# Kernel tuning notes

Hardware: AMD Instinct MI355X
Metric: run time of the kernel (lower is better)

Reference implementation:

```python
import jax, jax.numpy as jnp
import numpy as np

EMBED_DIM = 768
NUM_HEADS = 12
HEAD_DIM = EMBED_DIM // NUM_HEADS
SCALE = HEAD_DIM ** -0.5
B, N = 8, 1024


def setup_inputs() -> dict:
    key = jax.random.key(0)
    ks = jax.random.split(key, 5)
    return {
        "x": jax.random.normal(ks[0], (B, N, EMBED_DIM), dtype=jnp.float32),
        "qkv_w": jax.random.normal(ks[1], (3 * EMBED_DIM, EMBED_DIM), dtype=jnp.float32) * 0.02,
        "qkv_b": jax.random.normal(ks[2], (3 * EMBED_DIM,), dtype=jnp.float32) * 0.02,
        "proj_w": jax.random.normal(ks[3], (EMBED_DIM, EMBED_DIM), dtype=jnp.float32) * 0.02,
        "proj_b": jax.random.normal(ks[4], (EMBED_DIM,), dtype=jnp.float32) * 0.02,
    }


def reference(x, qkv_w, qkv_b, proj_w, proj_b):
    b, n, c = x.shape
    h, hd = NUM_HEADS, HEAD_DIM
    # QKV projection: [b,n,3c]
    qkv = jnp.einsum("bnc,dc->bnd", x, qkv_w) + qkv_b
    qkv = qkv.reshape(b, n, 3, h, hd).transpose(2, 0, 3, 1, 4)  # [3,b,h,n,hd]
    q, k, v = qkv[0], qkv[1], qkv[2]
    # scaled dot-product attention (eager path; dropout is identity in eval)
    attn = jnp.einsum("bhqd,bhkd->bhqk", q, k) * SCALE
    attn = jax.nn.softmax(attn, axis=-1)
    out = jnp.einsum("bhqk,bhkd->bhqd", attn, v)  # [b,h,n,hd]
    out = out.transpose(0, 2, 1, 3).reshape(b, n, c)
    # output projection
    return jnp.einsum("bnc,dc->bnd", out, proj_w) + proj_b
```

## Files before the change

kernel.cpp:

```cpp
#include <hip/hip_runtime.h>
#include <hip/hip_bf16.h>

typedef __attribute__((ext_vector_type(4))) float f32x4;
typedef __attribute__((ext_vector_type(16))) float f32x16;
typedef __attribute__((ext_vector_type(8))) short short8;
typedef unsigned short u16;

#define MFMA(a, b, c) __builtin_amdgcn_mfma_f32_16x16x32_bf16((a), (b), (c), 0, 0, 0)
#define MFMA32(a, b, c) __builtin_amdgcn_mfma_f32_32x32x16_bf16((a), (b), (c), 0, 0, 0)

#define WAITVM_BAR(N) do {                                          \
    asm volatile("s_waitcnt vmcnt(" #N ")" ::: "memory");           \
    __builtin_amdgcn_s_barrier();                                   \
    __builtin_amdgcn_sched_barrier(0);                              \
} while (0)
#define BAR2() do {                                                 \
    __builtin_amdgcn_sched_barrier(0);                              \
    __builtin_amdgcn_s_barrier();                                   \
    __builtin_amdgcn_sched_barrier(0);                              \
} while (0)

static constexpr int EMBED = 768;
static constexpr int NH = 12;
static constexpr int HD = 64;
static constexpr int BATCH = 8;
static constexpr int SEQ = 1024;

__device__ __forceinline__ u16 f2bu(float f) {
    __hip_bfloat16 h = __float2bfloat16(f);
    u16 u; __builtin_memcpy(&u, &h, 2); return u;
}
__device__ __forceinline__ float exp2a(float x) {
    float r; asm("v_exp_f32 %0, %1" : "=v"(r) : "v"(x)); return r;
}
__device__ __forceinline__ unsigned cvt_pk_bf16(float lo, float hi) {
    unsigned r; asm("v_cvt_pk_bf16_f32 %0, %1, %2" : "=v"(r) : "v"(lo), "v"(hi)); return r;
}
__device__ __forceinline__ float max3f(float a, float b, float c) {
    return fmaxf(fmaxf(a, b), c);
}
__device__ __forceinline__ void swap32(unsigned& a, unsigned& b) {
    asm volatile("v_permlane32_swap_b32 %0, %1" : "+v"(a), "+v"(b));
}
__device__ __forceinline__ short8 mk8(unsigned w0, unsigned w1, unsigned w2, unsigned w3) {
    union { unsigned u[4]; short8 s; } c;
    c.u[0] = w0; c.u[1] = w1; c.u[2] = w2; c.u[3] = w3;
    return c.s;
}

__global__ void cvt_all_k(const float* __restrict__ x, const float* __restrict__ w1,
                          const float* __restrict__ w2,
                          u16* __restrict__ xb, u16* __restrict__ wb, u16* __restrict__ pw) {
    const int n1 = BATCH * SEQ * EMBED;
    const int n2 = 3 * EMBED * EMBED;
    const int n3 = EMBED * EMBED;
    int i = (blockIdx.x * blockDim.x + threadIdx.x) * 4;
    const float* src; u16* dst;
    if (i < n1)            { src = x  + i;             dst = xb + i; }
    else if (i < n1 + n2)  { src = w1 + (i - n1);      dst = wb + (i - n1); }
    else if (i < n1+n2+n3) { src = w2 + (i - n1 - n2); dst = pw + (i - n1 - n2); }
    else return;
    float4 v = *reinterpret_cast<const float4*>(src);
    ushort4 o;
    o.x = f2bu(v.x); o.y = f2bu(v.y); o.z = f2bu(v.z); o.w = f2bu(v.w);
    *reinterpret_cast<ushort4*>(dst) = o;
}

template <int EPI>
__global__ __launch_bounds__(256)
void gemm_bt_k(const u16* __restrict__ A, const u16* __restrict__ Bw,
               const float* __restrict__ bias,
               u16* __restrict__ q_out, u16* __restrict__ k_out,
               u16* __restrict__ vt_out, float* __restrict__ f_out)
{
    __shared__ __attribute__((aligned(16))) char smem[65536];
    const int tid  = threadIdx.x;
    const int wave = tid >> 6, lane = tid & 63;
    const int hi   = lane >> 4, l15 = lane & 15;
    const int wr   = wave >> 1, wc = wave & 1;
    const int bm   = blockIdx.x, bn = blockIdx.y;

    f32x4 acc[4][4] = {};

    const size_t arow0 = (size_t)bm * 128;
    const size_t brow0 = (size_t)bn * 128;

    auto stage = [&](int buf, int kt) {
        char* Ab = smem + buf * 32768;
        char* Bb = Ab + 16384;
#pragma unroll
        for (int c = 0; c < 4; ++c) {
            int ck   = c * 4 + wave;
            int p    = ck * 1024 + lane * 16;
            int row  = p >> 7;
            int pcol = (p & 127) ^ ((row & 7) << 4);
            const u16* srcA = A  + (arow0 + row) * EMBED + kt + (pcol >> 1);
            const u16* srcB = Bw + (brow0 + row) * EMBED + kt + (pcol >> 1);
            __builtin_amdgcn_global_load_lds((const __attribute__((address_space(1))) void*)srcA,
                                             (__attribute__((address_space(3))) void*)(Ab + ck * 1024), 16, 0, 0);
            __builtin_amdgcn_global_load_lds((const __attribute__((address_space(1))) void*)srcB,
                                             (__attribute__((address_space(3))) void*)(Bb + ck * 1024), 16, 0, 0);
        }
    };

    auto comp = [&](const char* Ab, const char* Bb) {
#pragma unroll
        for (int kk = 0; kk < 2; ++kk) {
            short8 af[4], bf[4];
#pragma unroll
            for (int mi = 0; mi < 4; ++mi) {
                int R  = wr * 64 + mi * 16 + l15;
                int Cb = kk * 64 + hi * 16;
                af[mi] = *reinterpret_cast<const short8*>(Ab + R * 128 + (Cb ^ ((R & 7) << 4)));
            }
#pragma unroll
            for (int ni = 0; ni < 4; ++ni) {
                int R  = wc * 64 + ni * 16 + l15;
                int Cb = kk * 64 + hi * 16;
                bf[ni] = *reinterpret_cast<const short8*>(Bb + R * 128 + (Cb ^ ((R & 7) << 4)));
            }
#pragma unroll
            for (int mi = 0; mi < 4; ++mi)
#pragma unroll
                for (int ni = 0; ni < 4; ++ni)
                    acc[mi][ni] = MFMA(af[mi], bf[ni], acc[mi][ni]);
        }
    };

    const char* A0 = smem;
    const char* B0 = smem + 16384;
    const char* A1 = smem + 32768;
    const char* B1 = smem + 49152;

    stage(0, 0);
#pragma unroll
    for (int tt = 0; tt < 5; ++tt) {
        stage(1, (2 * tt + 1) * 64);
        WAITVM_BAR(8);
        comp(A0, B0);
        BAR2();
        stage(0, (2 * tt + 2) * 64);
        WAITVM_BAR(8);
        comp(A1, B1);
        BAR2();
    }
    stage(1, 11 * 64);
    WAITVM_BAR(8);
    comp(A0, B0);
    BAR2();
    WAITVM_BAR(0);
    comp(A1, B1);

#pragma unroll
    for (int mi = 0; mi < 4; ++mi) {
        int crow0 = bm * 128 + wr * 64 + mi * 16 + hi * 4;
#pragma unroll
        for (int ni = 0; ni < 4; ++ni) {
            int ccol = bn * 128 + wc * 64 + ni * 16 + l15;
            float bv = bias[ccol];
            if constexpr (EPI == 0) {
                int which = ccol / 768;
                int rem   = ccol - which * 768;
                int hh = rem >> 6, hd = rem & 63;
                int bb = crow0 >> 10, nn0 = crow0 & 1023;
                size_t bh = (size_t)(bb * NH + hh);
                if (which == 2) {
                    uint2 pk;
                    pk.x = cvt_pk_bf16(acc[mi][ni][0] + bv, acc[mi][ni][1] + bv);
                    pk.y = cvt_pk_bf16(acc[mi][ni][2] + bv, acc[mi][ni][3] + bv);
                    *reinterpret_cast<uint2*>(&vt_out[(bh * HD + hd) * SEQ + nn0]) = pk;
                } else if (which == 0) {
#pragma unroll
                    for (int r = 0; r < 4; ++r)
                        q_out[(bh * SEQ + nn0 + r) * HD + hd] =
                            f2bu((acc[mi][ni][r] + bv) * 0.18033688f);
                } else {
#pragma unroll
                    for (int r = 0; r < 4; ++r)
                        k_out[(bh * SEQ + nn0 + r) * HD + hd] = f2bu(acc[mi][ni][r] + bv);
                }
            } else {
#pragma unroll
                for (int r = 0; r < 4; ++r)
                    f_out[(size_t)(crow0 + r) * EMBED + ccol] = acc[mi][ni][r] + bv;
            }
        }
    }
}

__global__ __launch_bounds__(256, 3)
void attn_k(const u16* __restrict__ Q, const u16* __restrict__ K,
            const u16* __restrict__ Vt, u16* __restrict__ AO)
{
    __shared__ __attribute__((aligned(16))) u16 kv[3][8192];

    const int tid = threadIdx.x;
    const int w   = tid >> 6, lane = tid & 63;
    const int h   = lane >> 5, l31 = lane & 31;
    const int f   = blockIdx.x;
    const int xcd = f & 7, i = f >> 3;
    const int bh  = xcd * 12 + (i % 12);
    const int q0w = (i / 12) * 128 + w * 32;

    const u16* Qh = Q  + (size_t)bh * SEQ * HD;
    const u16* Kh = K  + (size_t)bh * SEQ * HD;
    const u16* Vh = Vt + (size_t)bh * HD * SEQ;

    short8 qf[4];
#pragma unroll
    for (int ds = 0; ds < 4; ++ds)
        qf[ds] = *reinterpret_cast<const short8*>(
            Qh + (size_t)(q0w + l31) * HD + ds * 16 + h * 8);
    __builtin_amdgcn_sched_barrier(0);

    const u16* sptr[4]; int doff[4]; int sadv[4];
#pragma unroll
    for (int c = 0; c < 4; ++c) {
        int ch = c * 4 + w;
        int mc = ch & 7;
        int p  = mc * 1024 + lane * 16;
        int row = p >> 7;
        int colb = (p & 127) ^ ((row & 7) << 4);
        if (ch < 8) { sptr[c] = Kh + (size_t)row * HD + (colb >> 1); sadv[c] = 64 * HD; doff[c] = mc * 512; }
        else        { sptr[c] = Vh + (size_t)row * SEQ + (colb >> 1); sadv[c] = 64;     doff[c] = 4096 + mc * 512; }
    }
    auto stage = [&](int buf, int t) {
#pragma unroll
        for (int c = 0; c < 4; ++c)
            __builtin_amdgcn_global_load_lds(
                (const __attribute__((address_space(1))) void*)(sptr[c] + (size_t)t * sadv[c]),
                (__attribute__((address_space(3))) void*)(&kv[buf][doff[c]]), 16, 0, 0);
    };

    stage(0, 0);
    stage(1, 1);

    f32x16 accO[2] = {};
    float m = 0.f, lp = 0.f;

    auto tile = [&](const u16* Kb, const u16* Vb, bool first) {
        f32x16 st[2] = {{0}, {0}};
        __builtin_amdgcn_s_setprio(1);
#pragma unroll
        for (int mf = 0; mf < 2; ++mf) {
            int R  = mf * 32 + l31;
            int sw = (R & 7) << 4;
#pragma unroll
            for (int ds = 0; ds < 4; ++ds) {
                short8 kf = *reinterpret_cast<const short8*>(
                    Kb + R * 64 + (((ds * 32 + h * 16) ^ sw) >> 1));
                st[mf] = MFMA32(kf, qf[ds], st[mf]);
            }
        }
        __builtin_amdgcn_s_setprio(0);

        float x0 = max3f(st[0][0],  st[0][1],  st[0][2]);
        float x1 = max3f(st[0][3],  st[0][4],  st[0][5]);
        float x2 = max3f(st[0][6],  st[0][7],  st[0][8]);
        float x3 = max3f(st[0][9],  st[0][10], st[0][11]);
        float x4 = max3f(st[0][12], st[0][13], st[0][14]);
        float x5 = max3f(st[0][15], st[1][0],  st[1][1]);
        float x6 = max3f(st[1][2],  st[1][3],  st[1][4]);
        float x7 = max3f(st[1][5],  st[1][6],  st[1][7]);
        float x8 = max3f(st[1][8],  st[1][9],  st[1][10]);
        float x9 = max3f(st[1][11], st[1][12], st[1][13]);
        float xa = fmaxf(st[1][14], st[1][15]);
        float y0 = max3f(x0, x1, x2);
        float y1 = max3f(x3, x4, x5);
        float y2 = max3f(x6, x7, x8);
        float y3 = fmaxf(x9, xa);
        float tm = fmaxf(max3f(y0, y1, y2), y3);
        tm = fmaxf(tm, __shfl_xor(tm, 32, 64));
        if (first) m = tm;

        unsigned pkw[2][8];
        float s0 = 0.f, s1 = 0.f;
#pragma unroll
        for (int mf = 0; mf < 2; ++mf)
#pragma unroll
            for (int p = 0; p < 8; ++p) {
                float e0 = exp2a(st[mf][2 * p]     - m);
                float e1 = exp2a(st[mf][2 * p + 1] - m);
                if (mf == 0) s0 += e0 + e1; else s1 += e0 + e1;
                pkw[mf][p] = cvt_pk_bf16(e0, e1);
            }
        lp += s0 + s1;

        short8 pb[4];
#pragma unroll
        for (int ks = 0; ks < 4; ++ks) {
            int mf = ks >> 1, b4 = (ks & 1) * 4;
            unsigned E0 = pkw[mf][b4 + 0], E1 = pkw[mf][b4 + 1];
            unsigned D0 = pkw[mf][b4 + 2], D1 = pkw[mf][b4 + 3];
            swap32(E0, D0);
            swap32(E1, D1);
            pb[ks] = mk8(E0, E1, D0, D1);
        }

        __builtin_amdgcn_s_setprio(1);
#pragma unroll
        for (int df = 0; df < 2; ++df) {
            int R  = df * 32 + l31;
            int sw = (R & 7) << 4;
#pragma unroll
            for (int ks = 0; ks < 4; ++ks) {
                short8 vf = *reinterpret_cast<const short8*>(
                    Vb + R * 64 + (((ks * 32 + h * 16) ^ sw) >> 1));
                accO[df] = MFMA32(vf, pb[ks], accO[df]);
            }
        }
        __builtin_amdgcn_s_setprio(0);

        if (!first && !__all(tm <= m + 8.f)) {
            float mn = fmaxf(m, tm);
            float s  = exp2a(m - mn);
            m = mn;
            lp *= s;
#pragma unroll
            for (int df = 0; df < 2; ++df)
#pragma unroll
                for (int r = 0; r < 16; ++r) accO[df][r] *= s;
        }
    };

    auto one = [&](int bc, int bs, int tn, bool ds, bool first) {
        asm volatile("s_waitcnt vmcnt(4)" ::: "memory");
        __builtin_amdgcn_s_barrier();
        __builtin_amdgcn_sched_barrier(0);
        if (ds) stage(bs, tn);
        tile(&kv[bc][0], &kv[bc][4096], first);
        __builtin_amdgcn_sched_barrier(0);
    };

    one(0, 2, 2, true, true);
    one(1, 0, 3, true, false);
    one(2, 1, 4, true, false);
    for (int g = 1; g < 5; ++g) {
        one(0, 2, 3 * g + 2, true, false);
        one(1, 0, 3 * g + 3, 3 * g + 3 <= 15, false);
        one(2, 1, 3 * g + 4, 3 * g + 4 <= 15, false);
    }
    asm volatile("s_waitcnt vmcnt(0)" ::: "memory");
    __builtin_amdgcn_s_barrier();
    __builtin_amdgcn_sched_barrier(0);
    tile(&kv[0][0], &kv[0][4096], false);

    lp += __shfl_xor(lp, 32, 64);
    float linv = 1.f / lp;
    const int bb = bh / NH, hh = bh - bb * NH;
    size_t rowb = ((size_t)bb * SEQ + q0w + l31) * EMBED + hh * HD;
#pragma unroll
    for (int df = 0; df < 2; ++df)
#pragma unroll
        for (int g = 0; g < 4; ++g) {
            float o0 = accO[df][4 * g + 0] * linv;
            float o1 = accO[df][4 * g + 1] * linv;
            float o2 = accO[df][4 * g + 2] * linv;
            float o3 = accO[df][4 * g + 3] * linv;
            uint2 pk;
            pk.x = cvt_pk_bf16(o0, o1);
            pk.y = cvt_pk_bf16(o2, o3);
            *reinterpret_cast<uint2*>(&AO[rowb + df * 32 + 8 * g + 4 * h]) = pk;
        }
}

extern "C" void kernel_launch(void* const* d_in, const int* in_sizes, int n_in,
                              void* d_out, int out_size, void* d_ws, size_t ws_size,
                              hipStream_t stream)
{
    const float* x      = (const float*)d_in[0];
    const float* qkv_w  = (const float*)d_in[1];
    const float* qkv_b  = (const float*)d_in[2];
    const float* proj_w = (const float*)d_in[3];
    const float* proj_b = (const float*)d_in[4];
    float* out = (float*)d_out;

    char* ws = (char*)d_ws;
    u16* xb  = (u16*)(ws);
    u16* wb  = (u16*)(ws + 12582912);
    u16* pw  = (u16*)(ws + 16121856);
    u16* qb  = (u16*)(ws + 17301504);
    u16* kb  = (u16*)(ws + 29884416);
    u16* vt  = (u16*)(ws + 42467328);
    u16* ao  = (u16*)(ws + 55050240);

    cvt_all_k<<<8448, 256, 0, stream>>>(x, qkv_w, proj_w, xb, wb, pw);

    gemm_bt_k<0><<<dim3(64, 18), 256, 0, stream>>>(xb, wb, qkv_b, qb, kb, vt, nullptr);
    attn_k<<<768, 256, 0, stream>>>(qb, kb, vt, ao);
    gemm_bt_k<1><<<dim3(64, 6), 256, 0, stream>>>(ao, pw, proj_b, nullptr, nullptr, nullptr, out);
}
```

Measured before the change: 103.9 us.

## Compute softmax row sums via MFMA with ones and precompute LDS offsets

Replaces the per-lane VALU accumulation of softmax denominators (and the cross-lane shuffle) with an extra MFMA that multiplies the bf16 probability fragments by a ones vector, so the row sum arrives in an accumulator. The initial running max is fixed at a constant rather than taken from the first tile, which removes the first-tile special case. Swizzled LDS read offsets in both the GEMM and attention kernels are hoisted out of the inner loops. The sum now uses bf16-rounded probabilities, which adds MFMA work per tile and changes rounding slightly.

```diff
diff --git a/kernel.cpp b/kernel.cpp
--- a/kernel.cpp
+++ b/kernel.cpp
@@ -103,22 +103,25 @@
         }
     };
 
-    auto comp = [&](const char* Ab, const char* Bb) {
+    const int sw_l = (l15 & 7) << 4;
+    int aoff[2], boff[2];
+#pragma unroll
+    for (int kk = 0; kk < 2; ++kk) {
+        int col = (kk * 64 + hi * 16) ^ sw_l;
+        aoff[kk] = (wr * 64 + l15) * 128 + col;
+        boff[kk] = (wc * 64 + l15) * 128 + col;
+    }
+
+    auto comp = [&](int buf) {
 #pragma unroll
         for (int kk = 0; kk < 2; ++kk) {
             short8 af[4], bf[4];
 #pragma unroll
-            for (int mi = 0; mi < 4; ++mi) {
-                int R  = wr * 64 + mi * 16 + l15;
-                int Cb = kk * 64 + hi * 16;
-                af[mi] = *reinterpret_cast<const short8*>(Ab + R * 128 + (Cb ^ ((R & 7) << 4)));
-            }
-#pragma unroll
-            for (int ni = 0; ni < 4; ++ni) {
-                int R  = wc * 64 + ni * 16 + l15;
-                int Cb = kk * 64 + hi * 16;
-                bf[ni] = *reinterpret_cast<const short8*>(Bb + R * 128 + (Cb ^ ((R & 7) << 4)));
-            }
+            for (int mi = 0; mi < 4; ++mi)
+                af[mi] = *reinterpret_cast<const short8*>(smem + buf * 32768 + aoff[kk] + mi * 2048);
+#pragma unroll
+            for (int ni = 0; ni < 4; ++ni)
+                bf[ni] = *reinterpret_cast<const short8*>(smem + buf * 32768 + 16384 + boff[kk] + ni * 2048);
 #pragma unroll
             for (int mi = 0; mi < 4; ++mi)
 #pragma unroll
@@ -126,30 +129,25 @@
                     acc[mi][ni] = MFMA(af[mi], bf[ni], acc[mi][ni]);
         }
     };
-
-    const char* A0 = smem;
-    const char* B0 = smem + 16384;
-    const char* A1 = smem + 32768;
-    const char* B1 = smem + 49152;
 
     stage(0, 0);
 #pragma unroll
     for (int tt = 0; tt < 5; ++tt) {
         stage(1, (2 * tt + 1) * 64);
         WAITVM_BAR(8);
-        comp(A0, B0);
+        comp(0);
         BAR2();
         stage(0, (2 * tt + 2) * 64);
         WAITVM_BAR(8);
-        comp(A1, B1);
+        comp(1);
         BAR2();
     }
     stage(1, 11 * 64);
     WAITVM_BAR(8);
-    comp(A0, B0);
+    comp(0);
     BAR2();
     WAITVM_BAR(0);
-    comp(A1, B1);
+    comp(1);
 
 #pragma unroll
     for (int mi = 0; mi < 4; ++mi) {
@@ -235,23 +233,31 @@
     stage(0, 0);
     stage(1, 1);
 
+    const int sw_l = (l31 & 7) << 4;
+    int koff[4];
+#pragma unroll
+    for (int ds = 0; ds < 4; ++ds)
+        koff[ds] = l31 * 128 + ((ds * 32 + h * 16) ^ sw_l);
+
+    union { unsigned u[4]; short8 s; } oc;
+    oc.u[0] = oc.u[1] = oc.u[2] = oc.u[3] = 0x3F803F80u;
+    const short8 ones8 = oc.s;
+
     f32x16 accO[2] = {};
-    float m = 0.f, lp = 0.f;
-
-    auto tile = [&](const u16* Kb, const u16* Vb, bool first) {
+    f32x16 lsum = {};
+    float m = 8.f;
+
+    auto tile = [&](int BC) {
+        const char* base = (const char*)kv + BC * 16384;
         f32x16 st[2] = {{0}, {0}};
         __builtin_amdgcn_s_setprio(1);
 #pragma unroll
-        for (int mf = 0; mf < 2; ++mf) {
-            int R  = mf * 32 + l31;
-            int sw = (R & 7) << 4;
+        for (int mf = 0; mf < 2; ++mf)
 #pragma unroll
             for (int ds = 0; ds < 4; ++ds) {
-                short8 kf = *reinterpret_cast<const short8*>(
-                    Kb + R * 64 + (((ds * 32 + h * 16) ^ sw) >> 1));
+                short8 kf = *reinterpret_cast<const short8*>(base + mf * 4096 + koff[ds]);
                 st[mf] = MFMA32(kf, qf[ds], st[mf]);
             }
-        }
         __builtin_amdgcn_s_setprio(0);
 
         float x0 = max3f(st[0][0],  st[0][1],  st[0][2]);
@@ -265,26 +271,19 @@
         float x8 = max3f(st[1][8],  st[1][9],  st[1][10]);
         float x9 = max3f(st[1][11], st[1][12], st[1][13]);
         float xa = fmaxf(st[1][14], st[1][15]);
-        float y0 = max3f(x0, x1, x2);
-        float y1 = max3f(x3, x4, x5);
-        float y2 = max3f(x6, x7, x8);
-        float y3 = fmaxf(x9, xa);
-        float tm = fmaxf(max3f(y0, y1, y2), y3);
+        float tm = fmaxf(max3f(max3f(x0, x1, x2), max3f(x3, x4, x5), max3f(x6, x7, x8)),
+                         max3f(x9, xa, -1e30f));
         tm = fmaxf(tm, __shfl_xor(tm, 32, 64));
-        if (first) m = tm;
 
         unsigned pkw[2][8];
-        float s0 = 0.f, s1 = 0.f;
 #pragma unroll
         for (int mf = 0; mf < 2; ++mf)
 #pragma unroll
             for (int p = 0; p < 8; ++p) {
                 float e0 = exp2a(st[mf][2 * p]     - m);
                 float e1 = exp2a(st[mf][2 * p + 1] - m);
-                if (mf == 0) s0 += e0 + e1; else s1 += e0 + e1;
                 pkw[mf][p] = cvt_pk_bf16(e0, e1);
             }
-        lp += s0 + s1;
 
         short8 pb[4];
 #pragma unroll
@@ -299,54 +298,51 @@
 
         __builtin_amdgcn_s_setprio(1);
 #pragma unroll
-        for (int df = 0; df < 2; ++df) {
-            int R  = df * 32 + l31;
-            int sw = (R & 7) << 4;
+        for (int ks = 0; ks < 4; ++ks)
+            lsum = MFMA32(ones8, pb[ks], lsum);
+#pragma unroll
+        for (int df = 0; df < 2; ++df)
 #pragma unroll
             for (int ks = 0; ks < 4; ++ks) {
-                short8 vf = *reinterpret_cast<const short8*>(
-                    Vb + R * 64 + (((ks * 32 + h * 16) ^ sw) >> 1));
+                short8 vf = *reinterpret_cast<const short8*>(base + 8192 + df * 4096 + koff[ks]);
                 accO[df] = MFMA32(vf, pb[ks], accO[df]);
             }
-        }
         __builtin_amdgcn_s_setprio(0);
 
-        if (!first && !__all(tm <= m + 8.f)) {
+        if (!__all(tm <= m + 8.f)) {
             float mn = fmaxf(m, tm);
             float s  = exp2a(m - mn);
             m = mn;
-            lp *= s;
-#pragma unroll
-            for (int df = 0; df < 2; ++df)
-#pragma unroll
-                for (int r = 0; r < 16; ++r) accO[df][r] *= s;
-        }
-    };
-
-    auto one = [&](int bc, int bs, int tn, bool ds, bool first) {
+#pragma unroll
+            for (int r = 0; r < 16; ++r) {
+                accO[0][r] *= s; accO[1][r] *= s; lsum[r] *= s;
+            }
+        }
+    };
+
+    auto one = [&](int bc, int bs, int tn, bool ds) {
         asm volatile("s_waitcnt vmcnt(4)" ::: "memory");
         __builtin_amdgcn_s_barrier();
         __builtin_amdgcn_sched_barrier(0);
         if (ds) stage(bs, tn);
-        tile(&kv[bc][0], &kv[bc][4096], first);
+        tile(bc);
         __builtin_amdgcn_sched_barrier(0);
     };
 
-    one(0, 2, 2, true, true);
-    one(1, 0, 3, true, false);
-    one(2, 1, 4, true, false);
+    one(0, 2, 2, true);
+    one(1, 0, 3, true);
+    one(2, 1, 4, true);
     for (int g = 1; g < 5; ++g) {
-        one(0, 2, 3 * g + 2, true, false);
-        one(1, 0, 3 * g + 3, 3 * g + 3 <= 15, false);
-        one(2, 1, 3 * g + 4, 3 * g + 4 <= 15, false);
+        one(0, 2, 3 * g + 2, true);
+        one(1, 0, 3 * g + 3, 3 * g + 3 <= 15);
+        one(2, 1, 3 * g + 4, 3 * g + 4 <= 15);
     }
     asm volatile("s_waitcnt vmcnt(0)" ::: "memory");
     __builtin_amdgcn_s_barrier();
     __builtin_amdgcn_sched_barrier(0);
-    tile(&kv[0][0], &kv[0][4096], false);
-
-    lp += __shfl_xor(lp, 32, 64);
-    float linv = 1.f / lp;
+    tile(0);
+
+    float linv = 1.f / lsum[0];
     const int bb = bh / NH, hh = bh - bb * NH;
     size_t rowb = ((size_t)bb * SEQ + q0w + l31) * EMBED + hh * HD;
 #pragma unroll
```

Measured after the change: 102.6 us. Within noise of the previous version (-1.3%).
